# Kernel optimization log

Measured on AMD Instinct MI355X. Metric: run time of the kernel, lower is better.

## Reference

```python
import jax, jax.numpy as jnp
import numpy as np

N, G, F, H, K, D = 131072, 512, 256, 128, 64, 8
# domain d owns global logit columns [d*K, (d+1)*K)
DOMAIN_COLS = np.arange(D * K, dtype=np.int32).reshape(D, K)


def setup_inputs() -> dict:
    key = jax.random.key(0)
    ks = jax.random.split(key, 6)
    z_base_global = jax.random.normal(ks[0], (N, G), jnp.float32)
    feats = jax.random.normal(ks[1], (N, F), jnp.float32)
    domain_ids = jax.random.randint(ks[2], (N,), 0, D)
    W1 = jax.random.normal(ks[3], (F + 3, H), jnp.float32) * 0.05  # trunk Linear
    b1 = jnp.zeros((H,), jnp.float32)
    W2 = jax.random.normal(ks[4], (H, K), jnp.float32) * 0.05      # head Linear (max_k = K)
    b2 = jnp.zeros((K,), jnp.float32)
    alphas = jnp.ones((D,), jnp.float32)                            # alpha_init = 1.0
    return dict(z_base_global=z_base_global, feats=feats, W1=W1, b1=b1,
                W2=W2, b2=b2, alphas=alphas, domain_ids=domain_ids)


def _conf_stats(local_logits):
    # matches get_conf_from_local_logits (torch.no_grad -> stop_gradient at call site)
    p = jax.nn.softmax(local_logits, axis=-1)
    p_max = jnp.max(p, axis=-1, keepdims=True)
    entropy = -jnp.sum(p * jnp.log(jnp.clip(p, 1e-12, None)), axis=-1, keepdims=True)
    top2 = jax.lax.top_k(p, 2)[0]
    margin = top2[:, :1] - top2[:, 1:2]
    return jnp.concatenate([p_max, entropy, margin], axis=-1)  # [N, 3]


def reference(z_base_global, feats, W1, b1, W2, b2, alphas, domain_ids):
    # per-row column set for its domain: [N, K]
    cols = jnp.asarray(DOMAIN_COLS)[domain_ids]
    # gather local logits (reads of the pre-update z, as in the torch loop)
    local_logits = jnp.take_along_axis(z_base_global, cols, axis=1)  # [N, K]
    c = jax.lax.stop_gradient(_conf_stats(local_logits))             # [N, 3]
    x = jnp.concatenate([feats, c], axis=-1)                         # [N, F+3]
    h = jax.nn.relu(x @ W1 + b1)                                     # trunk
    dz = (h @ W2 + b2) * alphas[domain_ids][:, None]                 # [N, K]
    rows = jnp.arange(z_base_global.shape[0])[:, None]
    # scatter-add residual deltas into the owned columns (index_put_ accumulate=True)
    return z_base_global.at[rows, cols].add(dz)
```

## Files before the change

### kernel.cpp

```cpp
#include <hip/hip_runtime.h>


typedef __attribute__((ext_vector_type(8))) short short8;
typedef __attribute__((ext_vector_type(4))) float f32x4;

#define NROWS_TOT 131072
#define G 512
#define F 256
#define HID 128
#define KW 64
#define MROWS 16
#define XROW 296
#define HROW 136
#define W1FRAG_ELEMS (9*8*64*8)
#define W2FRAG_ELEMS (4*4*64*8)

__device__ __forceinline__ unsigned short f2bf(float f) {
  unsigned u = __float_as_uint(f);
  u += 0x7FFFu + ((u >> 16) & 1u);
  return (unsigned short)(u >> 16);
}

__global__ void prep_kernel(const float* __restrict__ W1, const float* __restrict__ W2,
                            unsigned short* __restrict__ ws) {
  int f = blockIdx.x * 256 + threadIdx.x;
  if (f < W1FRAG_ELEMS) {
    int j = f & 7, lane = (f >> 3) & 63, tile = f >> 9;
    int nt = tile & 7, kc = tile >> 3;
    int k = kc * 32 + ((lane >> 4) << 3) + j;
    int n = (nt << 4) + (lane & 15);
    float v = (k < 259) ? W1[k * HID + n] : 0.0f;
    ws[f] = f2bf(v);
  } else {
    int f2 = f - W1FRAG_ELEMS;
    int j = f2 & 7, lane = (f2 >> 3) & 63, tile = f2 >> 9;
    int nt = tile & 3, kc = tile >> 2;
    int k = kc * 32 + ((lane >> 4) << 3) + j;
    int n = (nt << 4) + (lane & 15);
    ws[W1FRAG_ELEMS + f2] = f2bf(W2[k * KW + n]);
  }
}

__global__ __launch_bounds__(256, 6) void adapter_main(
    const float* __restrict__ z, const float* __restrict__ feats,
    const float* __restrict__ b1, const float* __restrict__ b2,
    const float* __restrict__ alphas, const int* __restrict__ dom_ids,
    const unsigned short* __restrict__ wfrag, float* __restrict__ out) {
  __shared__ unsigned short Xb[MROWS * XROW];
  __shared__ unsigned short Hb[MROWS * HROW];
  __shared__ float dzs[MROWS * KW];
  __shared__ float alph[MROWS];
  __shared__ int   doms[MROWS];

  const int tid  = threadIdx.x;
  const int lane = tid & 63;
  const int wv   = tid >> 6;
  const int l15  = lane & 15;
  const int quad = lane >> 4;
  const int r0   = blockIdx.x * MROWS;

  float4 zr[8];
  #pragma unroll
  for (int it = 0; it < 8; ++it) {
    int flat = it * 256 + tid;
    int row  = flat >> 7;
    int c4   = flat & 127;
    zr[it] = *(const float4*)&z[(size_t)(r0 + row) * G + c4 * 4];
  }

  {
    int rsub = tid >> 6;
    int c4   = tid & 63;
    #pragma unroll
    for (int i = 0; i < 4; ++i) {
      int row = i * 4 + rsub;
      const float4 v = *(const float4*)&feats[(size_t)(r0 + row) * F + c4 * 4];
      ushort4 p;
      p.x = f2bf(v.x); p.y = f2bf(v.y); p.z = f2bf(v.z); p.w = f2bf(v.w);
      *(ushort4*)&Xb[row * XROW + c4 * 4] = p;
    }
  }

  #pragma unroll
  for (int row = wv; row < MROWS; row += 4) {
    const int gr = r0 + row;
    const int d  = dom_ids[gr];
    float l = z[(size_t)gr * G + d * KW + lane];
    float m = l;
    #pragma unroll
    for (int off = 32; off; off >>= 1) m = fmaxf(m, __shfl_xor(m, off));
    float e = __expf(l - m);
    float S = e, wsum = e * (l - m);
    #pragma unroll
    for (int off = 32; off; off >>= 1) { S += __shfl_xor(S, off); wsum += __shfl_xor(wsum, off); }
    float l2 = (l < m) ? l : -1e30f;
    #pragma unroll
    for (int off = 32; off; off >>= 1) l2 = fmaxf(l2, __shfl_xor(l2, off));
    float inv    = 1.0f / S;
    float pmax   = inv;
    float ent    = __logf(S) - wsum * inv;
    float margin = (1.0f - __expf(l2 - m)) * inv;
    if (lane < 40) {
      float v = (lane == 0) ? pmax : (lane == 1) ? ent : (lane == 2) ? margin : 0.0f;
      Xb[row * XROW + 256 + lane] = f2bf(v);
    }
    if (lane == 0) { doms[row] = d; alph[row] = alphas[d]; }
  }
  __syncthreads();

  {
    const int ntb = wv * 2;
    f32x4 acc[2];
    acc[0] = f32x4{0.f, 0.f, 0.f, 0.f};
    acc[1] = f32x4{0.f, 0.f, 0.f, 0.f};
    const unsigned short* Arow = &Xb[l15 * XROW];
    const short8* Wp = (const short8*)wfrag;
    #pragma unroll
    for (int kc = 0; kc < 9; ++kc) {
      short8 a = *(const short8*)&Arow[kc * 32 + quad * 8];
      const short8* bp = Wp + (size_t)(kc * 8 + ntb) * 64 + lane;
      short8 bf0 = bp[0], bf1 = bp[64];
      acc[0] = __builtin_amdgcn_mfma_f32_16x16x32_bf16(a, bf0, acc[0], 0, 0, 0);
      acc[1] = __builtin_amdgcn_mfma_f32_16x16x32_bf16(a, bf1, acc[1], 0, 0, 0);
    }
    #pragma unroll
    for (int t = 0; t < 2; ++t) {
      int n = (ntb + t) * 16 + l15;
      float bias = b1[n];
      #pragma unroll
      for (int r = 0; r < 4; ++r) {
        int row = quad * 4 + r;
        Hb[row * HROW + n] = f2bf(fmaxf(acc[t][r] + bias, 0.f));
      }
    }
  }
  __syncthreads();

  {
    const int nt0 = wv;
    f32x4 acc2 = f32x4{0.f, 0.f, 0.f, 0.f};
    const unsigned short* Arow = &Hb[l15 * HROW];
    const short8* Wp = (const short8*)(wfrag + W1FRAG_ELEMS);
    #pragma unroll
    for (int kc = 0; kc < 4; ++kc) {
      short8 a = *(const short8*)&Arow[kc * 32 + quad * 8];
      const short8* bp = Wp + (kc * 4 + nt0) * 64 + lane;
      acc2 = __builtin_amdgcn_mfma_f32_16x16x32_bf16(a, bp[0], acc2, 0, 0, 0);
    }
    {
      int n = nt0 * 16 + l15;
      float bias = b2[n];
      #pragma unroll
      for (int r = 0; r < 4; ++r) {
        int row = quad * 4 + r;
        dzs[row * KW + n] = (acc2[r] + bias) * alph[row];
      }
    }
  }
  __syncthreads();

  #pragma unroll
  for (int it = 0; it < 8; ++it) {
    int flat = it * 256 + tid;
    int row  = flat >> 7;
    int c4   = flat & 127;
    size_t gidx = (size_t)(r0 + row) * G + c4 * 4;
    float4 v = zr[it];
    int off = c4 - doms[row] * 16;
    if ((unsigned)off < 16u) {
      const float4 dv = *(const float4*)&dzs[row * KW + off * 4];
      v.x += dv.x; v.y += dv.y; v.z += dv.z; v.w += dv.w;
    }
    *(float4*)&out[gidx] = v;
  }
}

extern "C" void kernel_launch(void* const* d_in, const int* in_sizes, int n_in,
                              void* d_out, int out_size, void* d_ws, size_t ws_size,
                              hipStream_t stream) {
  const float* z      = (const float*)d_in[0];
  const float* feats  = (const float*)d_in[1];
  const float* W1     = (const float*)d_in[2];
  const float* b1     = (const float*)d_in[3];
  const float* W2     = (const float*)d_in[4];
  const float* b2     = (const float*)d_in[5];
  const float* alphas = (const float*)d_in[6];
  const int*   dom    = (const int*)d_in[7];
  unsigned short* wfrag = (unsigned short*)d_ws;
  float* out = (float*)d_out;

  hipLaunchKernelGGL(prep_kernel, dim3(176), dim3(256), 0, stream, W1, W2, wfrag);
  hipLaunchKernelGGL(adapter_main, dim3(NROWS_TOT / MROWS), dim3(256), 0, stream,
                     z, feats, b1, b2, alphas, dom, wfrag, out);
}
```

Baseline: 572.9 us.

## Defer z tile load to epilogue, batch gathers, raise occupancy bound

The full z tile is now loaded only after the MLP stages instead of being held in 32 registers across the whole kernel. This frees registers so the launch bound can ask for 8 blocks per CU. The feats loads and the per-row domain/logit gathers are batched so several loads are in flight before they are used. The cost is that z is read twice (once for the logits, once in the epilogue) and its latency is no longer hidden behind the MLP compute, so the epilogue leans on higher occupancy and L2 hits to cover it.

```diff
diff --git a/kernel.cpp b/kernel.cpp
--- a/kernel.cpp
+++ b/kernel.cpp
@@ -41,7 +41,7 @@
   }
 }
 
-__global__ __launch_bounds__(256, 6) void adapter_main(
+__global__ __launch_bounds__(256, 8) void adapter_main(
     const float* __restrict__ z, const float* __restrict__ feats,
     const float* __restrict__ b1, const float* __restrict__ b2,
     const float* __restrict__ alphas, const int* __restrict__ dom_ids,
@@ -59,52 +59,58 @@
   const int quad = lane >> 4;
   const int r0   = blockIdx.x * MROWS;
 
-  float4 zr[8];
-  #pragma unroll
-  for (int it = 0; it < 8; ++it) {
-    int flat = it * 256 + tid;
-    int row  = flat >> 7;
-    int c4   = flat & 127;
-    zr[it] = *(const float4*)&z[(size_t)(r0 + row) * G + c4 * 4];
-  }
-
   {
     int rsub = tid >> 6;
     int c4   = tid & 63;
+    float4 fv[4];
     #pragma unroll
     for (int i = 0; i < 4; ++i) {
       int row = i * 4 + rsub;
-      const float4 v = *(const float4*)&feats[(size_t)(r0 + row) * F + c4 * 4];
+      fv[i] = *(const float4*)&feats[(size_t)(r0 + row) * F + c4 * 4];
+    }
+    #pragma unroll
+    for (int i = 0; i < 4; ++i) {
+      int row = i * 4 + rsub;
       ushort4 p;
-      p.x = f2bf(v.x); p.y = f2bf(v.y); p.z = f2bf(v.z); p.w = f2bf(v.w);
+      p.x = f2bf(fv[i].x); p.y = f2bf(fv[i].y); p.z = f2bf(fv[i].z); p.w = f2bf(fv[i].w);
       *(ushort4*)&Xb[row * XROW + c4 * 4] = p;
     }
   }
 
-  #pragma unroll
-  for (int row = wv; row < MROWS; row += 4) {
-    const int gr = r0 + row;
-    const int d  = dom_ids[gr];
-    float l = z[(size_t)gr * G + d * KW + lane];
-    float m = l;
-    #pragma unroll
-    for (int off = 32; off; off >>= 1) m = fmaxf(m, __shfl_xor(m, off));
-    float e = __expf(l - m);
-    float S = e, wsum = e * (l - m);
-    #pragma unroll
-    for (int off = 32; off; off >>= 1) { S += __shfl_xor(S, off); wsum += __shfl_xor(wsum, off); }
-    float l2 = (l < m) ? l : -1e30f;
-    #pragma unroll
-    for (int off = 32; off; off >>= 1) l2 = fmaxf(l2, __shfl_xor(l2, off));
-    float inv    = 1.0f / S;
-    float pmax   = inv;
-    float ent    = __logf(S) - wsum * inv;
-    float margin = (1.0f - __expf(l2 - m)) * inv;
-    if (lane < 40) {
-      float v = (lane == 0) ? pmax : (lane == 1) ? ent : (lane == 2) ? margin : 0.0f;
-      Xb[row * XROW + 256 + lane] = f2bf(v);
-    }
-    if (lane == 0) { doms[row] = d; alph[row] = alphas[d]; }
+  {
+    int dv[4];
+    float lv[4];
+    #pragma unroll
+    for (int i = 0; i < 4; ++i) dv[i] = dom_ids[r0 + wv + i * 4];
+    #pragma unroll
+    for (int i = 0; i < 4; ++i) {
+      int gr = r0 + wv + i * 4;
+      lv[i] = z[(size_t)gr * G + dv[i] * KW + lane];
+    }
+    #pragma unroll
+    for (int i = 0; i < 4; ++i) {
+      int row = wv + i * 4;
+      float l = lv[i];
+      float m = l;
+      #pragma unroll
+      for (int off = 32; off; off >>= 1) m = fmaxf(m, __shfl_xor(m, off));
+      float e = __expf(l - m);
+      float S = e, wsum = e * (l - m);
+      #pragma unroll
+      for (int off = 32; off; off >>= 1) { S += __shfl_xor(S, off); wsum += __shfl_xor(wsum, off); }
+      float l2 = (l < m) ? l : -1e30f;
+      #pragma unroll
+      for (int off = 32; off; off >>= 1) l2 = fmaxf(l2, __shfl_xor(l2, off));
+      float inv    = 1.0f / S;
+      float pmax   = inv;
+      float ent    = __logf(S) - wsum * inv;
+      float margin = (1.0f - __expf(l2 - m)) * inv;
+      if (lane < 40) {
+        float v = (lane == 0) ? pmax : (lane == 1) ? ent : (lane == 2) ? margin : 0.0f;
+        Xb[row * XROW + 256 + lane] = f2bf(v);
+      }
+      if (lane == 0) { doms[row] = dv[i]; alph[row] = alphas[dv[i]]; }
+    }
   }
   __syncthreads();
 
@@ -159,19 +165,29 @@
   }
   __syncthreads();
 
-  #pragma unroll
-  for (int it = 0; it < 8; ++it) {
-    int flat = it * 256 + tid;
-    int row  = flat >> 7;
-    int c4   = flat & 127;
-    size_t gidx = (size_t)(r0 + row) * G + c4 * 4;
-    float4 v = zr[it];
-    int off = c4 - doms[row] * 16;
-    if ((unsigned)off < 16u) {
-      const float4 dv = *(const float4*)&dzs[row * KW + off * 4];
-      v.x += dv.x; v.y += dv.y; v.z += dv.z; v.w += dv.w;
-    }
-    *(float4*)&out[gidx] = v;
+  {
+    float4 zv[8];
+    #pragma unroll
+    for (int it = 0; it < 8; ++it) {
+      int flat = it * 256 + tid;
+      int row  = flat >> 7;
+      int c4   = flat & 127;
+      zv[it] = *(const float4*)&z[(size_t)(r0 + row) * G + c4 * 4];
+    }
+    #pragma unroll
+    for (int it = 0; it < 8; ++it) {
+      int flat = it * 256 + tid;
+      int row  = flat >> 7;
+      int c4   = flat & 127;
+      size_t gidx = (size_t)(r0 + row) * G + c4 * 4;
+      float4 v = zv[it];
+      int off = c4 - doms[row] * 16;
+      if ((unsigned)off < 16u) {
+        const float4 dv = *(const float4*)&dzs[row * KW + off * 4];
+        v.x += dv.x; v.y += dv.y; v.z += dv.z; v.w += dv.w;
+      }
+      *(float4*)&out[gidx] = v;
+    }
   }
 }
 
```

Measured after the change: 526.1 us. -8.2%, faster.
